# Kernel tuning notes

Measured on AMD Instinct MI355X. Metric: run time of the kernel, lower is better.

## Reference

```python
import jax, jax.numpy as jnp
import numpy as np

B, S, D = 8, 2048, 768
N_SPANS = 512
MAX_W = 30  # static max span width (inclusive width in tokens)
H = 100
NEG = -1e30


def setup_inputs() -> dict:
    key = jax.random.key(0)
    k1, k2, k3, k4, k5, k6 = jax.random.split(key, 6)
    seq_tensor = jax.random.normal(k1, (B, S, D), dtype=jnp.float32)
    starts = jax.random.randint(k2, (B, N_SPANS), 0, S - MAX_W)
    widths = jax.random.randint(k3, (B, N_SPANS), 1, MAX_W + 1)  # span length in [1, MAX_W]
    ends_excl = starts + widths  # exclusive end, as module expects
    span_indices = jnp.stack([starts, ends_excl], axis=-1).astype(jnp.int64)
    span_mask = (jax.random.uniform(k4, (B, N_SPANS)) > 0.1).astype(jnp.int32)
    att_w = jax.random.normal(k5, (D, 1), dtype=jnp.float32) / np.sqrt(D)
    att_b = jnp.zeros((1,), dtype=jnp.float32)
    ffnn_w = jax.random.normal(k6, (D, H), dtype=jnp.float32) / np.sqrt(D)
    ffnn_b = jnp.zeros((H,), dtype=jnp.float32)
    return {"seq_tensor": seq_tensor, "span_indices": span_indices, "span_mask": span_mask,
            "att_w": att_w, "att_b": att_b, "ffnn_w": ffnn_w, "ffnn_b": ffnn_b}


def reference(seq_tensor, span_indices, span_mask, att_w, att_b, ffnn_w, ffnn_b):
    # exclusive end -> inclusive end (span_end_is_exclusive=True)
    starts = span_indices[..., 0]
    ends = span_indices[..., 1] - 1
    widths = ends - starts  # inclusive width - 1, in [0, MAX_W-1]

    offsets = jnp.arange(MAX_W)  # [W]
    raw_idx = starts[..., None] + offsets  # [B, N, W]
    width_mask = offsets <= widths[..., None]  # [B, N, W]
    idx = jnp.where(width_mask, raw_idx, 0)

    # global attention logits over the sequence: [B, S]
    att_logits = (jnp.einsum('bsd,do->bso', seq_tensor, att_w) + att_b)[..., 0]

    # gather span token embeddings and logits: [B, N, W, D], [B, N, W]
    span_emb = jax.vmap(lambda seq, i: seq[i])(seq_tensor, idx)
    span_logits = jax.vmap(lambda lg, i: lg[i])(att_logits, idx)

    # masked softmax over span width
    span_logits = jnp.where(width_mask, span_logits, NEG)
    attn = jax.nn.softmax(span_logits, axis=-1)  # [B, N, W]

    attended = jnp.einsum('bnw,bnwd->bnd', attn, span_emb)  # [B, N, D]
    attended = attended * span_mask.astype(attended.dtype)[..., None]

    # FeedForward: 1 layer Linear + tanh (dropout=0)
    out = jnp.tanh(jnp.einsum('bnd,dh->bnh', attended, ffnn_w) + ffnn_b)
    return out
```

## Files before the change

kernel.cpp:

```cpp
#include <hip/hip_runtime.h>
#include <cstdint>
#include <cstddef>

#define NB 8
#define NS 2048
#define ND 768
#define NSP 512
#define MAXW 30
#define NH 100
#define LDP 104
#define NKS (ND / 32)

typedef __attribute__((ext_vector_type(8))) short short8;
typedef __attribute__((ext_vector_type(4))) float floatx4;

__device__ inline unsigned short f2bf(float f) {
    unsigned u = __float_as_uint(f);
    return (unsigned short)((u + 0x7fffu + ((u >> 16) & 1u)) >> 16);
}
__device__ inline float bf2f(unsigned short h) {
    return __uint_as_float(((unsigned)h) << 16);
}

union PackUS { unsigned short us[8]; uint4 v; short8 s8; };

__global__ __launch_bounds__(256) void pack_b_kernel(
    const float* __restrict__ ffnn_w, const float* __restrict__ att_w,
    uint4* __restrict__ Bfrag)
{
    int ks = blockIdx.x;
    for (int idx = threadIdx.x; idx < 8 * 64; idx += 256) {
        int cf = idx >> 6, lane = idx & 63;
        int q = lane >> 4, r = lane & 15;
        int n = cf * 16 + r;
        PackUS p;
#pragma unroll
        for (int j = 0; j < 8; j++) {
            int k = ks * 32 + q * 8 + j;
            float v = (n < NH) ? ffnn_w[(size_t)k * NH + n]
                               : (n == NH ? att_w[k] : 0.f);
            p.us[j] = f2bf(v);
        }
        Bfrag[(size_t)(ks * 8 + cf) * 64 + lane] = p.v;
    }
}

__device__ inline void split8(const float* x, short8& hi, short8& lo) {
    PackUS ph, pl;
#pragma unroll
    for (int i = 0; i < 8; i++) {
        unsigned short h = f2bf(x[i]);
        ph.us[i] = h;
        pl.us[i] = f2bf(x[i] - bf2f(h));
    }
    hi = ph.s8;
    lo = pl.s8;
}

__global__ __launch_bounds__(256) void proj_kernel(
    const float* __restrict__ seq, const uint4* __restrict__ Bfrag,
    float* __restrict__ P)
{
    const int t = threadIdx.x;
    const int wave = t >> 6, lane = t & 63;
    const int q = lane >> 4, r = lane & 15;
    const int rf = wave >> 1;
    const int cfbase = (wave & 1) * 4;
    const int row0 = blockIdx.x * 32 + rf * 16;

    floatx4 acc[4] = {{0.f, 0.f, 0.f, 0.f}, {0.f, 0.f, 0.f, 0.f},
                      {0.f, 0.f, 0.f, 0.f}, {0.f, 0.f, 0.f, 0.f}};

    const float* arow = seq + (size_t)(row0 + r) * ND + q * 8;

#pragma unroll 2
    for (int ks = 0; ks < NKS; ++ks) {
        float av[8];
        *(float4*)&av[0] = *(const float4*)(arow + ks * 32);
        *(float4*)&av[4] = *(const float4*)(arow + ks * 32 + 4);
        short8 ahi, alo;
        split8(av, ahi, alo);
#pragma unroll
        for (int c = 0; c < 4; ++c) {
            PackUS pb;
            pb.v = Bfrag[(size_t)(ks * 8 + cfbase + c) * 64 + lane];
            acc[c] = __builtin_amdgcn_mfma_f32_16x16x32_bf16(ahi, pb.s8, acc[c], 0, 0, 0);
            acc[c] = __builtin_amdgcn_mfma_f32_16x16x32_bf16(alo, pb.s8, acc[c], 0, 0, 0);
        }
    }

#pragma unroll
    for (int c = 0; c < 4; ++c) {
        int col = (cfbase + c) * 16 + r;
        if (col <= NH) {
#pragma unroll
            for (int reg = 0; reg < 4; ++reg)
                P[(size_t)(row0 + q * 4 + reg) * LDP + col] = acc[c][reg];
        }
    }
}

__global__ __launch_bounds__(256) void span_kernel(
    const int* __restrict__ span_idx, const int* __restrict__ span_mask,
    const float* __restrict__ P, const float* __restrict__ ffnn_b,
    float* __restrict__ out)
{
    const int wave = threadIdx.x >> 6, lane = threadIdx.x & 63;
    const int gs = blockIdx.x * 4 + wave;
    const int b = gs / NSP;
    const int st = span_idx[2 * gs];
    int w = span_idx[2 * gs + 1] - st;
    w = max(1, min(w, MAXW));

    const float* Pb = P + ((size_t)b * NS + st) * LDP;

    float lg = (lane < w) ? Pb[lane * LDP + NH] : -1e30f;
    float mx = lg;
#pragma unroll
    for (int off = 32; off > 0; off >>= 1) mx = fmaxf(mx, __shfl_xor(mx, off));
    float e = (lane < w) ? expf(lg - mx) : 0.f;
    float sum = e;
#pragma unroll
    for (int off = 32; off > 0; off >>= 1) sum += __shfl_xor(sum, off);
    float attn = e / sum;

    float acc0 = 0.f, acc1 = 0.f;
#pragma unroll
    for (int i = 0; i < MAXW; ++i) {
        float a = __shfl(attn, i);
        const float* Pr = Pb + i * LDP;
        acc0 += a * Pr[lane];
        if (lane < NH - 64) acc1 += a * Pr[64 + lane];
    }

    float m = (float)span_mask[gs];
    out[(size_t)gs * NH + lane] = tanhf(m * acc0 + ffnn_b[lane]);
    if (lane < NH - 64)
        out[(size_t)gs * NH + 64 + lane] = tanhf(m * acc1 + ffnn_b[64 + lane]);
}

extern "C" void kernel_launch(void* const* d_in, const int* in_sizes, int n_in,
                              void* d_out, int out_size, void* d_ws, size_t ws_size,
                              hipStream_t stream) {
    const float* seq      = (const float*)d_in[0];
    const int*   span_idx = (const int*)d_in[1];
    const int*   span_msk = (const int*)d_in[2];
    const float* att_w    = (const float*)d_in[3];
    const float* ffnn_w   = (const float*)d_in[5];
    const float* ffnn_b   = (const float*)d_in[6];
    float* out = (float*)d_out;

    float* P = (float*)d_ws;
    uint4* Bfrag = (uint4*)((char*)d_ws + (size_t)NB * NS * LDP * 4);

    pack_b_kernel<<<NKS, 256, 0, stream>>>(ffnn_w, att_w, Bfrag);
    proj_kernel<<<(NB * NS) / 32, 256, 0, stream>>>(seq, Bfrag, P);
    span_kernel<<<(NB * NSP) / 4, 256, 0, stream>>>(span_idx, span_msk, P, ffnn_b, out);
}
```

Baseline: 126.7 us.

## Retile projection GEMM, cheapen bf16 split, store logits contiguously, vectorize span gather

The projection kernel now processes 16 rows per block, with each wave computing two column fragments over the same A rows. It adds an occupancy hint. The float-to-bf16 hi/lo split becomes a bitmask truncation with residual instead of rounding each half. Attention logits are written to a separate contiguous array, so the span kernel reads them in one coalesced load. The span kernel uses float4 loads over the 100 output columns and fast exp. This trades redundant A reads across waves for more blocks and fewer ALU ops per element.

```diff
diff --git a/kernel.cpp b/kernel.cpp
--- a/kernel.cpp
+++ b/kernel.cpp
@@ -14,15 +14,21 @@
 typedef __attribute__((ext_vector_type(8))) short short8;
 typedef __attribute__((ext_vector_type(4))) float floatx4;
 
+union U4S8 { uint4 v; short8 s8; unsigned u[4]; unsigned short us[8]; };
+
 __device__ inline unsigned short f2bf(float f) {
     unsigned u = __float_as_uint(f);
     return (unsigned short)((u + 0x7fffu + ((u >> 16) & 1u)) >> 16);
 }
-__device__ inline float bf2f(unsigned short h) {
-    return __uint_as_float(((unsigned)h) << 16);
+
+__device__ inline void split2(float x0, float x1, unsigned& hi, unsigned& lo) {
+    unsigned u0 = __float_as_uint(x0), u1 = __float_as_uint(x1);
+    unsigned h0 = u0 & 0xFFFF0000u, h1 = u1 & 0xFFFF0000u;
+    hi = (u0 >> 16) | h1;
+    float r0 = x0 - __uint_as_float(h0);
+    float r1 = x1 - __uint_as_float(h1);
+    lo = (__float_as_uint(r0) >> 16) | (__float_as_uint(r1) & 0xFFFF0000u);
 }
-
-union PackUS { unsigned short us[8]; uint4 v; short8 s8; };
 
 __global__ __launch_bounds__(256) void pack_b_kernel(
     const float* __restrict__ ffnn_w, const float* __restrict__ att_w,
@@ -33,7 +39,7 @@
         int cf = idx >> 6, lane = idx & 63;
         int q = lane >> 4, r = lane & 15;
         int n = cf * 16 + r;
-        PackUS p;
+        U4S8 p;
 #pragma unroll
         for (int j = 0; j < 8; j++) {
             int k = ks * 32 + q * 8 + j;
@@ -45,65 +51,60 @@
     }
 }
 
-__device__ inline void split8(const float* x, short8& hi, short8& lo) {
-    PackUS ph, pl;
-#pragma unroll
-    for (int i = 0; i < 8; i++) {
-        unsigned short h = f2bf(x[i]);
-        ph.us[i] = h;
-        pl.us[i] = f2bf(x[i] - bf2f(h));
-    }
-    hi = ph.s8;
-    lo = pl.s8;
-}
-
-__global__ __launch_bounds__(256) void proj_kernel(
+__global__ __launch_bounds__(256, 4) void proj_kernel(
     const float* __restrict__ seq, const uint4* __restrict__ Bfrag,
-    float* __restrict__ P)
+    float* __restrict__ P, float* __restrict__ Lg)
 {
     const int t = threadIdx.x;
     const int wave = t >> 6, lane = t & 63;
     const int q = lane >> 4, r = lane & 15;
-    const int rf = wave >> 1;
-    const int cfbase = (wave & 1) * 4;
-    const int row0 = blockIdx.x * 32 + rf * 16;
+    const int cf0 = wave * 2;
+    const int row0 = blockIdx.x * 16;
 
-    floatx4 acc[4] = {{0.f, 0.f, 0.f, 0.f}, {0.f, 0.f, 0.f, 0.f},
-                      {0.f, 0.f, 0.f, 0.f}, {0.f, 0.f, 0.f, 0.f}};
+    floatx4 acc[2] = {{0.f, 0.f, 0.f, 0.f}, {0.f, 0.f, 0.f, 0.f}};
 
     const float* arow = seq + (size_t)(row0 + r) * ND + q * 8;
+    const uint4* bptr = Bfrag + (size_t)cf0 * 64 + lane;
 
 #pragma unroll 2
     for (int ks = 0; ks < NKS; ++ks) {
-        float av[8];
-        *(float4*)&av[0] = *(const float4*)(arow + ks * 32);
-        *(float4*)&av[4] = *(const float4*)(arow + ks * 32 + 4);
-        short8 ahi, alo;
-        split8(av, ahi, alo);
-#pragma unroll
-        for (int c = 0; c < 4; ++c) {
-            PackUS pb;
-            pb.v = Bfrag[(size_t)(ks * 8 + cfbase + c) * 64 + lane];
-            acc[c] = __builtin_amdgcn_mfma_f32_16x16x32_bf16(ahi, pb.s8, acc[c], 0, 0, 0);
-            acc[c] = __builtin_amdgcn_mfma_f32_16x16x32_bf16(alo, pb.s8, acc[c], 0, 0, 0);
-        }
+        float4 f0 = *(const float4*)(arow + ks * 32);
+        float4 f1 = *(const float4*)(arow + ks * 32 + 4);
+        U4S8 b0, b1;
+        b0.v = bptr[(size_t)ks * 8 * 64];
+        b1.v = bptr[(size_t)ks * 8 * 64 + 64];
+
+        U4S8 hi, lo;
+        split2(f0.x, f0.y, hi.u[0], lo.u[0]);
+        split2(f0.z, f0.w, hi.u[1], lo.u[1]);
+        split2(f1.x, f1.y, hi.u[2], lo.u[2]);
+        split2(f1.z, f1.w, hi.u[3], lo.u[3]);
+
+        acc[0] = __builtin_amdgcn_mfma_f32_16x16x32_bf16(hi.s8, b0.s8, acc[0], 0, 0, 0);
+        acc[0] = __builtin_amdgcn_mfma_f32_16x16x32_bf16(lo.s8, b0.s8, acc[0], 0, 0, 0);
+        acc[1] = __builtin_amdgcn_mfma_f32_16x16x32_bf16(hi.s8, b1.s8, acc[1], 0, 0, 0);
+        acc[1] = __builtin_amdgcn_mfma_f32_16x16x32_bf16(lo.s8, b1.s8, acc[1], 0, 0, 0);
     }
 
 #pragma unroll
-    for (int c = 0; c < 4; ++c) {
-        int col = (cfbase + c) * 16 + r;
-        if (col <= NH) {
+    for (int c = 0; c < 2; ++c) {
+        int col = (cf0 + c) * 16 + r;
+        if (col < NH) {
 #pragma unroll
             for (int reg = 0; reg < 4; ++reg)
                 P[(size_t)(row0 + q * 4 + reg) * LDP + col] = acc[c][reg];
+        } else if (col == NH) {
+#pragma unroll
+            for (int reg = 0; reg < 4; ++reg)
+                Lg[row0 + q * 4 + reg] = acc[c][reg];
         }
     }
 }
 
 __global__ __launch_bounds__(256) void span_kernel(
     const int* __restrict__ span_idx, const int* __restrict__ span_mask,
-    const float* __restrict__ P, const float* __restrict__ ffnn_b,
-    float* __restrict__ out)
+    const float* __restrict__ P, const float* __restrict__ Lg,
+    const float* __restrict__ ffnn_b, float* __restrict__ out)
 {
     const int wave = threadIdx.x >> 6, lane = threadIdx.x & 63;
     const int gs = blockIdx.x * 4 + wave;
@@ -112,31 +113,37 @@
     int w = span_idx[2 * gs + 1] - st;
     w = max(1, min(w, MAXW));
 
-    const float* Pb = P + ((size_t)b * NS + st) * LDP;
-
-    float lg = (lane < w) ? Pb[lane * LDP + NH] : -1e30f;
+    float lg = -1e30f;
+    if (lane < w) lg = Lg[b * NS + st + lane];
     float mx = lg;
 #pragma unroll
     for (int off = 32; off > 0; off >>= 1) mx = fmaxf(mx, __shfl_xor(mx, off));
-    float e = (lane < w) ? expf(lg - mx) : 0.f;
+    float e = (lane < w) ? __expf(lg - mx) : 0.f;
     float sum = e;
 #pragma unroll
     for (int off = 32; off > 0; off >>= 1) sum += __shfl_xor(sum, off);
     float attn = e / sum;
 
-    float acc0 = 0.f, acc1 = 0.f;
+    int cl = min(lane, 24);
+    const float4* Pb4 = (const float4*)(P + ((size_t)b * NS + st) * LDP) + cl;
+    float4 acc = {0.f, 0.f, 0.f, 0.f};
 #pragma unroll
     for (int i = 0; i < MAXW; ++i) {
         float a = __shfl(attn, i);
-        const float* Pr = Pb + i * LDP;
-        acc0 += a * Pr[lane];
-        if (lane < NH - 64) acc1 += a * Pr[64 + lane];
+        float4 v = Pb4[i * (LDP / 4)];
+        acc.x += a * v.x; acc.y += a * v.y; acc.z += a * v.z; acc.w += a * v.w;
     }
 
-    float m = (float)span_mask[gs];
-    out[(size_t)gs * NH + lane] = tanhf(m * acc0 + ffnn_b[lane]);
-    if (lane < NH - 64)
-        out[(size_t)gs * NH + 64 + lane] = tanhf(m * acc1 + ffnn_b[64 + lane]);
+    if (lane < 25) {
+        float m = (float)span_mask[gs];
+        float4 bias = ((const float4*)ffnn_b)[lane];
+        float4 o;
+        o.x = tanhf(m * acc.x + bias.x);
+        o.y = tanhf(m * acc.y + bias.y);
+        o.z = tanhf(m * acc.z + bias.z);
+        o.w = tanhf(m * acc.w + bias.w);
+        *(float4*)(out + (size_t)gs * NH + 4 * lane) = o;
+    }
 }
 
 extern "C" void kernel_launch(void* const* d_in, const int* in_sizes, int n_in,
@@ -150,10 +157,12 @@
     const float* ffnn_b   = (const float*)d_in[6];
     float* out = (float*)d_out;
 
-    float* P = (float*)d_ws;
-    uint4* Bfrag = (uint4*)((char*)d_ws + (size_t)NB * NS * LDP * 4);
+    char* ws = (char*)d_ws;
+    float* P     = (float*)ws;
+    uint4* Bfrag = (uint4*)(ws + (size_t)NB * NS * LDP * 4);
+    float* Lg    = (float*)(ws + (size_t)NB * NS * LDP * 4 + (size_t)NKS * 8 * 64 * 16);
 
     pack_b_kernel<<<NKS, 256, 0, stream>>>(ffnn_w, att_w, Bfrag);
-    proj_kernel<<<(NB * NS) / 32, 256, 0, stream>>>(seq, Bfrag, P);
-    span_kernel<<<(NB * NSP) / 4, 256, 0, stream>>>(span_idx, span_msk, P, ffnn_b, out);
+    proj_kernel<<<(NB * NS) / 16, 256, 0, stream>>>(seq, Bfrag, P, Lg);
+    span_kernel<<<(NB * NSP) / 4, 256, 0, stream>>>(span_idx, span_msk, P, Lg, ffnn_b, out);
 }
```

Measured after the change: 127.9 us. No clear change (+1.0%).
